# Kernel optimization log

Hardware: AMD Instinct MI355X
Metric: run time of the kernel (lower is better)

## Reference

```python
import jax, jax.numpy as jnp
import numpy as np
import math

L = 192
D = 128
H = 12
C = 24
EPS = 1e-5


def _layernorm(x, w, b):
    mu = jnp.mean(x, axis=-1, keepdims=True)
    var = jnp.var(x, axis=-1, keepdims=True)
    return (x - mu) * jax.lax.rsqrt(var + EPS) * w + b


def setup_inputs() -> dict:
    key = jax.random.key(0)
    ks = jax.random.split(key, 8)
    s = 0.02
    return {
        "z_": jax.random.normal(ks[0], (L, L, D), dtype=jnp.float32),
        "ln_w": jnp.ones((D,), jnp.float32),
        "ln_b": jnp.zeros((D,), jnp.float32),
        "Wq": jax.random.normal(ks[1], (D, H * C), jnp.float32) * s,
        "bq": jnp.zeros((H * C,), jnp.float32),
        "Wk": jax.random.normal(ks[2], (D, H * C), jnp.float32) * s,
        "bk": jnp.zeros((H * C,), jnp.float32),
        "Wv": jax.random.normal(ks[3], (D, H * C), jnp.float32) * s,
        "bv": jnp.zeros((H * C,), jnp.float32),
        "Wb": jax.random.normal(ks[4], (D, H), jnp.float32) * s,
        "bb": jnp.zeros((H,), jnp.float32),
        "Wg": jax.random.normal(ks[5], (D, H * C), jnp.float32) * s,
        "bg": jnp.zeros((H * C,), jnp.float32),
        "Wo": jax.random.normal(ks[6], (H * C, D), jnp.float32) * s,
        "bo": jnp.zeros((D,), jnp.float32),
    }


def reference(z_, ln_w, ln_b, Wq, bq, Wk, bk, Wv, bv, Wb, bb, Wg, bg, Wo, bo):
    sq_c = 1.0 / math.sqrt(C)
    z = _layernorm(z_, ln_w, ln_b)                     # [L, L, D]
    q = (z @ Wq + bq).reshape(L, L, H, C)
    k = (z @ Wk + bk).reshape(L, L, H, C)
    v = (z @ Wv + bv).reshape(L, L, H, C)
    bias = z @ Wb + bb                                 # [L, L, H]
    # att[b, l, kk, h] = sum_c q[b, l, h, c] * k[kk, b_==l? no: kk, b, h, c]
    att = jnp.einsum('blhc,kbhc->blkh', q, k) * sq_c
    # torch: b[None].permute(0,2,1,3) -> add bias[kk, l, h] broadcast over b
    att = att + jnp.transpose(bias, (1, 0, 2))[None, :, :, :]
    att = jax.nn.softmax(att, axis=2)
    o = jnp.einsum('blkh,klhc->blhc', att, v)          # [L, L, H, C]
    g = jax.nn.sigmoid((z @ Wg + bg).reshape(L, L, H, C))
    o = (g * o).reshape(L, L, H * C)
    return o @ Wo + bo
```

## Files before the change

### kernel.cpp

```cpp
#include <hip/hip_runtime.h>
#include <hip/hip_bf16.h>
#include <math.h>

typedef __hip_bfloat16 bf16;
typedef unsigned short u16;
typedef unsigned int u32;
typedef __attribute__((ext_vector_type(8))) short bf16x8;
typedef __attribute__((ext_vector_type(4))) float f32x4;

#define LL 36864

__device__ __forceinline__ float wave_sum(float v) {
#pragma unroll
  for (int m = 32; m; m >>= 1) v += __shfl_xor(v, m, 64);
  return v;
}

__device__ __forceinline__ float bf2f(u16 u) {
  union { float f; u32 u; } c; c.u = ((u32)u) << 16; return c.f;
}
__device__ __forceinline__ u16 f2bf(float f) {
  union { float f; u32 u; } c; c.f = f;
  u32 r = c.u + 0x7fffu + ((c.u >> 16) & 1u);
  return (u16)(r >> 16);
}

__global__ __launch_bounds__(256) void k_cvt(const float* __restrict__ Wq,
                                             const float* __restrict__ Wk,
                                             const float* __restrict__ Wv,
                                             const float* __restrict__ Wg,
                                             bf16* __restrict__ Wcat) {
  int u = blockIdx.x * 256 + threadIdx.x;
  if (u >= 18432) return;
  int jg = u >> 4, k0 = (u & 15) * 8;
  int sec = jg / 288, j = jg % 288;
  const float* W = sec == 0 ? Wq : sec == 1 ? Wk : sec == 2 ? Wv : Wg;
  u16 pk[8];
#pragma unroll
  for (int i = 0; i < 8; ++i) pk[i] = f2bf(W[(size_t)(k0 + i) * 288 + j]);
  *reinterpret_cast<uint4*>(&Wcat[(size_t)jg * 128 + k0]) = *reinterpret_cast<uint4*>(pk);
}

__global__ __launch_bounds__(256) void k_cvt2(const float* __restrict__ Wo,
                                              bf16* __restrict__ Wot) {
  int u = blockIdx.x * 256 + threadIdx.x;
  if (u >= 4608) return;
  int n = u / 36, k0 = (u % 36) * 8;
  u16 pk[8];
#pragma unroll
  for (int i = 0; i < 8; ++i) pk[i] = f2bf(Wo[(size_t)(k0 + i) * 128 + n]);
  *reinterpret_cast<uint4*>(&Wot[(size_t)n * 288 + k0]) = *reinterpret_cast<uint4*>(pk);
}

__global__ __launch_bounds__(256) void k_ln(const float* __restrict__ zin,
                                            const float* __restrict__ w_,
                                            const float* __restrict__ b_,
                                            bf16* __restrict__ zb) {
  int t = threadIdx.x;
  int wv = t >> 6, lane = t & 63;
  size_t m = (size_t)blockIdx.x * 4 + wv;
  const float2 v = *reinterpret_cast<const float2*>(&zin[m * 128 + lane * 2]);
  float s = wave_sum(v.x + v.y);
  float ss = wave_sum(v.x * v.x + v.y * v.y);
  float mean = s * (1.0f / 128.0f);
  float var = ss * (1.0f / 128.0f) - mean * mean;
  float rs = rsqrtf(var + 1e-5f);
  float o0 = (v.x - mean) * rs * w_[lane * 2] + b_[lane * 2];
  float o1 = (v.y - mean) * rs * w_[lane * 2 + 1] + b_[lane * 2 + 1];
  u32 pk = (u32)f2bf(o0) | ((u32)f2bf(o1) << 16);
  *reinterpret_cast<u32*>(&zb[m * 128 + lane * 2]) = pk;
}

__global__ __launch_bounds__(256) void k_bias(const bf16* __restrict__ zb,
                                              const float* __restrict__ Wb,
                                              const float* __restrict__ bbv,
                                              float* __restrict__ biasb) {
  int t = threadIdx.x;
  int w = t >> 6, lane = t & 63;
  int c15 = lane & 15, g = lane >> 4;
  int m0 = (blockIdx.x * 4 + w) * 16;
  f32x4 acc = (f32x4){0.f, 0.f, 0.f, 0.f};
#pragma unroll
  for (int kt = 0; kt < 4; ++kt) {
    bf16x8 a = *reinterpret_cast<const bf16x8*>(
        &zb[(size_t)(m0 + c15) * 128 + kt * 32 + g * 8]);
    u16 bp[8];
#pragma unroll
    for (int j = 0; j < 8; ++j)
      bp[j] = (c15 < 12) ? f2bf(Wb[(size_t)(kt * 32 + g * 8 + j) * 12 + c15]) : (u16)0;
    bf16x8 b = *reinterpret_cast<bf16x8*>(bp);
    acc = __builtin_amdgcn_mfma_f32_16x16x32_bf16(a, b, acc, 0, 0, 0);
  }
  if (c15 < 12) {
    int kk = m0 / 192, l0 = m0 % 192;
    int p = (kk & 15) * 12 + (kk >> 4);
    float bv = bbv[c15];
#pragma unroll
    for (int i = 0; i < 4; ++i) {
      int l = l0 + 4 * g + i;
      biasb[(size_t)c15 * LL + (size_t)l * 192 + p] = acc[i] + bv;
    }
  }
}

__global__ __launch_bounds__(256) void k_proj(const bf16* __restrict__ zb,
    const bf16* __restrict__ Wcat,
    const float* __restrict__ bq, const float* __restrict__ bk,
    const float* __restrict__ bv, const float* __restrict__ bg,
    bf16* __restrict__ q2, bf16* __restrict__ k2,
    bf16* __restrict__ vb, bf16* __restrict__ gbuf) {
  __shared__ __align__(16) u16 Sb[192 * 104];
  int t = threadIdx.x;
  int w = t >> 6, lane = t & 63;
  int c15 = lane & 15, g = lane >> 4;
  int wm = w & 1, wn = w >> 1;
  int bx = blockIdx.x, y = blockIdx.y;
  int sec = y / 3, h0 = (y % 3) * 4;
  int m0 = bx * 192;
  int jbase = y * 96;
  f32x4 acc[6][3];
#pragma unroll
  for (int mt = 0; mt < 6; ++mt)
#pragma unroll
    for (int nt = 0; nt < 3; ++nt) acc[mt][nt] = (f32x4){0.f, 0.f, 0.f, 0.f};
#pragma unroll
  for (int kt = 0; kt < 4; ++kt) {
    bf16x8 a[6], b[3];
#pragma unroll
    for (int mt = 0; mt < 6; ++mt)
      a[mt] = *reinterpret_cast<const bf16x8*>(
          &zb[(size_t)(m0 + wm * 96 + mt * 16 + c15) * 128 + kt * 32 + g * 8]);
#pragma unroll
    for (int nt = 0; nt < 3; ++nt)
      b[nt] = *reinterpret_cast<const bf16x8*>(
          &Wcat[(size_t)(jbase + wn * 48 + nt * 16 + c15) * 128 + kt * 32 + g * 8]);
#pragma unroll
    for (int mt = 0; mt < 6; ++mt)
#pragma unroll
      for (int nt = 0; nt < 3; ++nt)
        acc[mt][nt] = __builtin_amdgcn_mfma_f32_16x16x32_bf16(a[mt], b[nt], acc[mt][nt], 0, 0, 0);
  }
  const float* barr = sec == 0 ? bq : sec == 1 ? bk : sec == 2 ? bv : bg;
#pragma unroll
  for (int nt = 0; nt < 3; ++nt) {
    int col = wn * 48 + nt * 16 + c15;
    float bval = barr[(y % 3) * 96 + col];
#pragma unroll
    for (int mt = 0; mt < 6; ++mt) {
      int rbase = wm * 96 + mt * 16 + 4 * g;
#pragma unroll
      for (int i = 0; i < 4; ++i)
        Sb[(rbase + i) * 104 + col] = f2bf(acc[mt][nt][i] + bval);
    }
  }
  __syncthreads();
  if (sec == 0) {
    bf16* dst0 = q2 + ((size_t)bx * 12 + h0) * 4608;
    for (int u = t; u < 2304; u += 256) {
      int hl = u / 576, off = (u % 576) * 8;
      int ml = off / 24, c0 = off % 24;
      uint4 val = *reinterpret_cast<const uint4*>(&Sb[ml * 104 + hl * 24 + c0]);
      *reinterpret_cast<uint4*>(&dst0[(size_t)hl * 4608 + off]) = val;
    }
  } else if (sec == 3) {
    for (int u = t; u < 2304; u += 256) {
      int ml = u / 12, col = (u % 12) * 8;
      uint4 val = *reinterpret_cast<const uint4*>(&Sb[ml * 104 + col]);
      *reinterpret_cast<uint4*>(&gbuf[(size_t)(m0 + ml) * 288 + h0 * 24 + col]) = val;
    }
  } else {
    bf16* dst = (sec == 1) ? k2 : vb;
    for (int u = t; u < 2304; u += 256) {
      int hl = u / 576, off = (u % 576) * 8;
      int ml = off / 24, c0 = off % 24;
      uint4 val = *reinterpret_cast<const uint4*>(&Sb[ml * 104 + hl * 24 + c0]);
      *reinterpret_cast<uint4*>(
          &dst[(((size_t)ml * 12 + h0 + hl) * 192 + bx) * 24 + c0]) = val;
    }
  }
}

__global__ __launch_bounds__(256) void k_attpv(const bf16* __restrict__ q2,
    const bf16* __restrict__ k2, const float* __restrict__ biasb,
    const bf16* __restrict__ vbuf, const bf16* __restrict__ gbuf,
    bf16* __restrict__ Patt, const bf16* __restrict__ Ppv,
    bf16* __restrict__ ogb, int la0, int lp0, int NT, int NL) {
  __shared__ __align__(16) char ldsraw[25600];
  int t = threadIdx.x;
  int w = t >> 6, lane = t & 63;
  int c15 = lane & 15, g = lane >> 4;
  const float sq_c = 0.20412414523193154f;
  bool is_att = (la0 >= 0) && (lp0 < 0 || blockIdx.z == 0);
  if (is_att) {
    int x = blockIdx.x, h = blockIdx.y;
    if (x >= 48) return;
    int bq = x * 4 + w;
    int lbase = la0 + blockIdx.z * NT * 16;
    u16* Sb = reinterpret_cast<u16*>(ldsraw) + (size_t)w * 3200;
    const bf16* ks = &k2[((size_t)bq * 12 + h) * 4608];
    const float* bsrc = &biasb[(size_t)h * LL];
    for (int lt = 0; lt < NT; ++lt) {
      int l0 = lbase + lt * 16;
      const bf16* qs = &q2[(((size_t)bq * 12 + h) * 192 + l0) * 24];
      bf16x8 afr = {0, 0, 0, 0, 0, 0, 0, 0};
      if (g < 3) afr = *reinterpret_cast<const bf16x8*>(&qs[c15 * 24 + g * 8]);
      f32x4 acc[12];
#pragma unroll
      for (int ct = 0; ct < 12; ++ct) {
        bf16x8 bfr = {0, 0, 0, 0, 0, 0, 0, 0};
        if (g < 3) bfr = *reinterpret_cast<const bf16x8*>(&ks[(ct * 16 + c15) * 24 + g * 8]);
        acc[ct] = __builtin_amdgcn_mfma_f32_16x16x32_bf16(afr, bfr, (f32x4){0.f, 0.f, 0.f, 0.f}, 0, 0, 0);
      }
#pragma unroll
      for (int i = 0; i < 4; ++i) {
        const float* bT = &bsrc[(size_t)(l0 + 4 * g + i) * 192 + c15 * 12];
        float4 b0 = *reinterpret_cast<const float4*>(&bT[0]);
        float4 b1 = *reinterpret_cast<const float4*>(&bT[4]);
        float4 b2 = *reinterpret_cast<const float4*>(&bT[8]);
        float bb12[12] = {b0.x, b0.y, b0.z, b0.w, b1.x, b1.y, b1.z, b1.w,
                          b2.x, b2.y, b2.z, b2.w};
#pragma unroll
        for (int ct = 0; ct < 12; ++ct)
          acc[ct][i] = acc[ct][i] * sq_c + bb12[ct];
      }
      float inv[4];
#pragma unroll
      for (int i = 0; i < 4; ++i) {
        float mx = -1e30f;
#pragma unroll
        for (int ct = 0; ct < 12; ++ct) mx = fmaxf(mx, acc[ct][i]);
#pragma unroll
        for (int msk = 1; msk < 16; msk <<= 1) mx = fmaxf(mx, __shfl_xor(mx, msk, 64));
        float sm = 0.f;
#pragma unroll
        for (int ct = 0; ct < 12; ++ct) {
          float e = __expf(acc[ct][i] - mx);
          acc[ct][i] = e;
          sm += e;
        }
#pragma unroll
        for (int msk = 1; msk < 16; msk <<= 1) sm += __shfl_xor(sm, msk, 64);
        inv[i] = 1.0f / sm;
      }
#pragma unroll
      for (int i = 0; i < 4; ++i)
#pragma unroll
        for (int ct = 0; ct < 12; ++ct)
          Sb[(4 * g + i) * 200 + ct * 16 + c15] = f2bf(acc[ct][i] * inv[i]);
      int lrel = l0 - la0;
      for (int u = lane; u < 384; u += 64) {
        int lloc = u / 24, oct = u % 24;
        uint4 val = *reinterpret_cast<const uint4*>(&Sb[lloc * 200 + oct * 8]);
        *reinterpret_cast<uint4*>(
            &Patt[(((size_t)(lrel + lloc) * 12 + h) * 192 + bq) * 192 + oct * 8]) = val;
      }
    }
  } else {
    if (lp0 < 0) return;
    int x = blockIdx.x, h = blockIdx.y;
    if (x >= NL) return;
    u16* Vt = reinterpret_cast<u16*>(ldsraw);
    float* Ob = reinterpret_cast<float*>(ldsraw + 12800) + (size_t)w * 416;
    int l = lp0 + x;
    int lrel = x;
    const bf16* vs = &vbuf[((size_t)l * 12 + h) * 4608];
    for (int u = t; u < 576; u += 256) {
      int kk = u / 3, c0 = (u % 3) * 8;
      uint4 val = *reinterpret_cast<const uint4*>(&vs[kk * 24 + c0]);
      const u16* pv = reinterpret_cast<const u16*>(&val);
#pragma unroll
      for (int i = 0; i < 8; ++i) Vt[(c0 + i) * 200 + kk] = pv[i];
    }
    __syncthreads();
    bf16x8 bfr[6][2];
#pragma unroll
    for (int kt = 0; kt < 6; ++kt)
#pragma unroll
      for (int nt = 0; nt < 2; ++nt)
        bfr[kt][nt] = *reinterpret_cast<const bf16x8*>(
            &Vt[(nt * 16 + c15) * 200 + kt * 32 + g * 8]);
    const bf16* Ps = &Ppv[((size_t)lrel * 12 + h) * 36864];
#pragma unroll
    for (int mi = 0; mi < 3; ++mi) {
      int mt = w * 3 + mi;
      f32x4 acc0 = (f32x4){0.f, 0.f, 0.f, 0.f};
      f32x4 acc1 = (f32x4){0.f, 0.f, 0.f, 0.f};
#pragma unroll
      for (int kt = 0; kt < 6; ++kt) {
        bf16x8 a = *reinterpret_cast<const bf16x8*>(
            &Ps[(size_t)(mt * 16 + c15) * 192 + kt * 32 + g * 8]);
        acc0 = __builtin_amdgcn_mfma_f32_16x16x32_bf16(a, bfr[kt][0], acc0, 0, 0, 0);
        acc1 = __builtin_amdgcn_mfma_f32_16x16x32_bf16(a, bfr[kt][1], acc1, 0, 0, 0);
      }
#pragma unroll
      for (int i = 0; i < 4; ++i) {
        Ob[(4 * g + i) * 26 + c15] = acc0[i];
        if (c15 < 8) Ob[(4 * g + i) * 26 + 16 + c15] = acc1[i];
      }
      if (lane < 48) {
        int r = lane / 3, c0 = (lane % 3) * 8;
        int b = mt * 16 + r;
        size_t m = (size_t)b * 192 + l;
        uint4 gv4 = *reinterpret_cast<const uint4*>(&gbuf[m * 288 + h * 24 + c0]);
        const u16* gp = reinterpret_cast<const u16*>(&gv4);
        u16 opk[8];
#pragma unroll
        for (int i = 0; i < 8; ++i) {
          float av = Ob[r * 26 + c0 + i];
          float sg = 1.0f / (1.0f + __expf(-bf2f(gp[i])));
          opk[i] = f2bf(av * sg);
        }
        *reinterpret_cast<uint4*>(&ogb[m * 288 + h * 24 + c0]) = *reinterpret_cast<uint4*>(opk);
      }
    }
  }
}

__global__ __launch_bounds__(256) void k_out(const bf16* __restrict__ ogb,
                                             const bf16* __restrict__ Wot,
                                             const float* __restrict__ bo,
                                             float* __restrict__ out) {
  int t = threadIdx.x;
  int w = t >> 6, lane = t & 63;
  int c15 = lane & 15, g = lane >> 4;
  int m0 = blockIdx.x * 64;
  int mrow = m0 + w * 16 + c15;
  f32x4 acc[8];
#pragma unroll
  for (int nt = 0; nt < 8; ++nt) acc[nt] = (f32x4){0.f, 0.f, 0.f, 0.f};
#pragma unroll
  for (int kt = 0; kt < 9; ++kt) {
    bf16x8 a = *reinterpret_cast<const bf16x8*>(&ogb[(size_t)mrow * 288 + kt * 32 + g * 8]);
    bf16x8 b[8];
#pragma unroll
    for (int nt = 0; nt < 8; ++nt)
      b[nt] = *reinterpret_cast<const bf16x8*>(&Wot[(size_t)(nt * 16 + c15) * 288 + kt * 32 + g * 8]);
#pragma unroll
    for (int nt = 0; nt < 8; ++nt)
      acc[nt] = __builtin_amdgcn_mfma_f32_16x16x32_bf16(a, b[nt], acc[nt], 0, 0, 0);
  }
#pragma unroll
  for (int nt = 0; nt < 8; ++nt) {
    int n = nt * 16 + c15;
    float bval = bo[n];
#pragma unroll
    for (int i = 0; i < 4; ++i) {
      int m = m0 + w * 16 + 4 * g + i;
      out[(size_t)m * 128 + n] = acc[nt][i] + bval;
    }
  }
}

extern "C" void kernel_launch(void* const* d_in, const int* in_sizes, int n_in,
                              void* d_out, int out_size, void* d_ws, size_t ws_size,
                              hipStream_t stream) {
  const float* z_in = (const float*)d_in[0];
  const float* ln_w = (const float*)d_in[1];
  const float* ln_b = (const float*)d_in[2];
  const float* Wq   = (const float*)d_in[3];
  const float* bq   = (const float*)d_in[4];
  const float* Wk   = (const float*)d_in[5];
  const float* bk   = (const float*)d_in[6];
  const float* Wv   = (const float*)d_in[7];
  const float* bv   = (const float*)d_in[8];
  const float* Wb   = (const float*)d_in[9];
  const float* bb   = (const float*)d_in[10];
  const float* Wg   = (const float*)d_in[11];
  const float* bg   = (const float*)d_in[12];
  const float* Wo   = (const float*)d_in[13];
  const float* bo   = (const float*)d_in[14];
  float* out = (float*)d_out;

  char* ws = (char*)d_ws;

  if (ws_size >= 256573440ull) {
    bf16* q2    = (bf16*)(ws + 0);
    bf16* ogb   = (bf16*)(ws + 0);
    bf16* k2    = (bf16*)(ws + 21233664);
    bf16* vb    = (bf16*)(ws + 42467328);
    bf16* gbuf  = (bf16*)(ws + 63700992);
    float* biasb = (float*)(ws + 84934656);
    bf16* P     = (bf16*)(ws + 86704128);
    bf16* zb    = (bf16*)(ws + 86704128);
    bf16* Wcat  = (bf16*)(ws + 96141312);
    bf16* Wot   = (bf16*)(ws + 86704128);

    k_cvt<<<dim3(72), dim3(256), 0, stream>>>(Wq, Wk, Wv, Wg, Wcat);
    k_ln<<<dim3(9216), dim3(256), 0, stream>>>(z_in, ln_w, ln_b, zb);
    k_bias<<<dim3(576), dim3(256), 0, stream>>>(zb, Wb, bb, biasb);
    k_proj<<<dim3(192, 12), dim3(256), 0, stream>>>(zb, Wcat, bq, bk, bv, bg,
                                                    q2, k2, vb, gbuf);
    k_attpv<<<dim3(48, 12, 4), dim3(256), 0, stream>>>(
        q2, k2, biasb, vb, gbuf, P, P, ogb, 0, -1, 3, 192);
    k_attpv<<<dim3(192, 12, 1), dim3(256), 0, stream>>>(
        q2, k2, biasb, vb, gbuf, P, P, ogb, -1, 0, 12, 192);
    k_cvt2<<<dim3(18), dim3(256), 0, stream>>>(Wo, Wot);
    k_out<<<dim3(576), dim3(256), 0, stream>>>(ogb, Wot, bo, out);
    return;
  }

  bf16* q2    = (bf16*)(ws + 0);
  bf16* k2    = (bf16*)(ws + 21233664);
  bf16* vb    = (bf16*)(ws + 42467328);
  bf16* gbuf  = (bf16*)(ws + 63700992);
  bf16* ogb   = (bf16*)(ws + 84934656);
  bf16* zb    = (bf16*)(ws + 84934656);
  bf16* Wcat  = (bf16*)(ws + 94371840);
  float* biasb = (float*)(ws + 106168320);
  char* Pbase = ws + 107937792;
  bf16* Wot   = (bf16*)(ws + 107937792);

  k_cvt<<<dim3(72), dim3(256), 0, stream>>>(Wq, Wk, Wv, Wg, Wcat);
  k_ln<<<dim3(9216), dim3(256), 0, stream>>>(z_in, ln_w, ln_b, zb);
  k_bias<<<dim3(576), dim3(256), 0, stream>>>(zb, Wb, bb, biasb);
  k_proj<<<dim3(192, 12), dim3(256), 0, stream>>>(zb, Wcat, bq, bk, bv, bg,
                                                  q2, k2, vb, gbuf);
  const size_t PB = 107937792ull;
  int CL;
  if      (ws_size >= PB + 84934656ull)  CL = 48;
  else if (ws_size >= PB + 56623104ull)  CL = 32;
  else if (ws_size >= PB + 28311552ull)  CL = 16;
  else                                   CL = -16;
  if (CL > 0) {
    int nch = 192 / CL;
    size_t csz = (size_t)CL * 884736ull;
    bf16* P0 = (bf16*)Pbase;
    bf16* P1 = (bf16*)(Pbase + csz);
    int NT = CL / 16;
    for (int n = 0; n <= nch; ++n) {
      bf16* Pa = (n & 1) ? P1 : P0;
      bf16* Pp = ((n - 1) & 1) ? P1 : P0;
      int la = (n < nch) ? n * CL : -1;
      int lp = (n >= 1) ? (n - 1) * CL : -1;
      if (la >= 0 && lp >= 0)
        k_attpv<<<dim3(48 > CL ? 48 : CL, 12, 2), dim3(256), 0, stream>>>(
            q2, k2, biasb, vb, gbuf, Pa, Pp, ogb, la, lp, NT, CL);
      else if (la >= 0)
        k_attpv<<<dim3(48, 12, 1), dim3(256), 0, stream>>>(
            q2, k2, biasb, vb, gbuf, Pa, Pp, ogb, la, -1, NT, CL);
      else
        k_attpv<<<dim3(CL, 12, 1), dim3(256), 0, stream>>>(
            q2, k2, biasb, vb, gbuf, Pa, Pp, ogb, -1, lp, NT, CL);
    }
  } else {
    bf16* P0 = (bf16*)Pbase;
    for (int n = 0; n < 12; ++n) {
      k_attpv<<<dim3(48, 12, 1), dim3(256), 0, stream>>>(
          q2, k2, biasb, vb, gbuf, P0, P0, ogb, n * 16, -1, 1, 16);
      k_attpv<<<dim3(16, 12, 1), dim3(256), 0, stream>>>(
          q2, k2, biasb, vb, gbuf, P0, P0, ogb, -1, n * 16, 1, 16);
    }
  }
  k_cvt2<<<dim3(18), dim3(256), 0, stream>>>(Wo, Wot);
  k_out<<<dim3(576), dim3(256), 0, stream>>>(ogb, Wot, bo, out);
}
```

Baseline: 225.4 us.

## Pipeline attention and PV in three 64-row chunks with multi-slice launches

Removes the large-workspace path that computed the full attention matrix in one launch, then PV in a second. It is replaced by a chunked pipeline of 64-row chunks with two buffers. Attention for the next chunk runs in the same launch as PV for the previous chunk, with the split set by a new ZA parameter on the z dimension. The goal is to overlap the two phases, keep P traffic in a smaller working set, and cut the number of launches compared with the smaller-chunk paths. It needs a slightly different workspace threshold and adds fill and drain launches.

```diff
diff --git a/kernel.cpp b/kernel.cpp
--- a/kernel.cpp
+++ b/kernel.cpp
@@ -184,13 +184,13 @@
     const bf16* __restrict__ k2, const float* __restrict__ biasb,
     const bf16* __restrict__ vbuf, const bf16* __restrict__ gbuf,
     bf16* __restrict__ Patt, const bf16* __restrict__ Ppv,
-    bf16* __restrict__ ogb, int la0, int lp0, int NT, int NL) {
+    bf16* __restrict__ ogb, int la0, int lp0, int NT, int NL, int ZA) {
   __shared__ __align__(16) char ldsraw[25600];
   int t = threadIdx.x;
   int w = t >> 6, lane = t & 63;
   int c15 = lane & 15, g = lane >> 4;
   const float sq_c = 0.20412414523193154f;
-  bool is_att = (la0 >= 0) && (lp0 < 0 || blockIdx.z == 0);
+  bool is_att = ((int)blockIdx.z < ZA);
   if (is_att) {
     int x = blockIdx.x, h = blockIdx.y;
     if (x >= 48) return;
@@ -372,33 +372,6 @@
   float* out = (float*)d_out;
 
   char* ws = (char*)d_ws;
-
-  if (ws_size >= 256573440ull) {
-    bf16* q2    = (bf16*)(ws + 0);
-    bf16* ogb   = (bf16*)(ws + 0);
-    bf16* k2    = (bf16*)(ws + 21233664);
-    bf16* vb    = (bf16*)(ws + 42467328);
-    bf16* gbuf  = (bf16*)(ws + 63700992);
-    float* biasb = (float*)(ws + 84934656);
-    bf16* P     = (bf16*)(ws + 86704128);
-    bf16* zb    = (bf16*)(ws + 86704128);
-    bf16* Wcat  = (bf16*)(ws + 96141312);
-    bf16* Wot   = (bf16*)(ws + 86704128);
-
-    k_cvt<<<dim3(72), dim3(256), 0, stream>>>(Wq, Wk, Wv, Wg, Wcat);
-    k_ln<<<dim3(9216), dim3(256), 0, stream>>>(z_in, ln_w, ln_b, zb);
-    k_bias<<<dim3(576), dim3(256), 0, stream>>>(zb, Wb, bb, biasb);
-    k_proj<<<dim3(192, 12), dim3(256), 0, stream>>>(zb, Wcat, bq, bk, bv, bg,
-                                                    q2, k2, vb, gbuf);
-    k_attpv<<<dim3(48, 12, 4), dim3(256), 0, stream>>>(
-        q2, k2, biasb, vb, gbuf, P, P, ogb, 0, -1, 3, 192);
-    k_attpv<<<dim3(192, 12, 1), dim3(256), 0, stream>>>(
-        q2, k2, biasb, vb, gbuf, P, P, ogb, -1, 0, 12, 192);
-    k_cvt2<<<dim3(18), dim3(256), 0, stream>>>(Wo, Wot);
-    k_out<<<dim3(576), dim3(256), 0, stream>>>(ogb, Wot, bo, out);
-    return;
-  }
-
   bf16* q2    = (bf16*)(ws + 0);
   bf16* k2    = (bf16*)(ws + 21233664);
   bf16* vb    = (bf16*)(ws + 42467328);
@@ -409,46 +382,60 @@
   float* biasb = (float*)(ws + 106168320);
   char* Pbase = ws + 107937792;
   bf16* Wot   = (bf16*)(ws + 107937792);
+  const size_t PB = 107937792ull;
 
   k_cvt<<<dim3(72), dim3(256), 0, stream>>>(Wq, Wk, Wv, Wg, Wcat);
   k_ln<<<dim3(9216), dim3(256), 0, stream>>>(z_in, ln_w, ln_b, zb);
   k_bias<<<dim3(576), dim3(256), 0, stream>>>(zb, Wb, bb, biasb);
   k_proj<<<dim3(192, 12), dim3(256), 0, stream>>>(zb, Wcat, bq, bk, bv, bg,
                                                   q2, k2, vb, gbuf);
-  const size_t PB = 107937792ull;
-  int CL;
-  if      (ws_size >= PB + 84934656ull)  CL = 48;
-  else if (ws_size >= PB + 56623104ull)  CL = 32;
-  else if (ws_size >= PB + 28311552ull)  CL = 16;
-  else                                   CL = -16;
-  if (CL > 0) {
-    int nch = 192 / CL;
-    size_t csz = (size_t)CL * 884736ull;
+
+  if (ws_size >= PB + 113246208ull) {
     bf16* P0 = (bf16*)Pbase;
-    bf16* P1 = (bf16*)(Pbase + csz);
-    int NT = CL / 16;
-    for (int n = 0; n <= nch; ++n) {
-      bf16* Pa = (n & 1) ? P1 : P0;
-      bf16* Pp = ((n - 1) & 1) ? P1 : P0;
-      int la = (n < nch) ? n * CL : -1;
-      int lp = (n >= 1) ? (n - 1) * CL : -1;
-      if (la >= 0 && lp >= 0)
-        k_attpv<<<dim3(48 > CL ? 48 : CL, 12, 2), dim3(256), 0, stream>>>(
-            q2, k2, biasb, vb, gbuf, Pa, Pp, ogb, la, lp, NT, CL);
-      else if (la >= 0)
+    bf16* P1 = (bf16*)(Pbase + 56623104);
+    k_attpv<<<dim3(48, 12, 2), dim3(256), 0, stream>>>(
+        q2, k2, biasb, vb, gbuf, P0, P0, ogb, 0, -1, 2, 0, 2);
+    k_attpv<<<dim3(64, 12, 3), dim3(256), 0, stream>>>(
+        q2, k2, biasb, vb, gbuf, P1, P0, ogb, 64, 0, 2, 64, 2);
+    k_attpv<<<dim3(64, 12, 3), dim3(256), 0, stream>>>(
+        q2, k2, biasb, vb, gbuf, P0, P1, ogb, 128, 64, 2, 64, 2);
+    k_attpv<<<dim3(64, 12, 1), dim3(256), 0, stream>>>(
+        q2, k2, biasb, vb, gbuf, P0, P0, ogb, -1, 128, 0, 64, 0);
+  } else {
+    int CL;
+    if      (ws_size >= PB + 84934656ull)  CL = 48;
+    else if (ws_size >= PB + 56623104ull)  CL = 32;
+    else if (ws_size >= PB + 28311552ull)  CL = 16;
+    else                                   CL = -16;
+    if (CL > 0) {
+      int nch = 192 / CL;
+      size_t csz = (size_t)CL * 884736ull;
+      bf16* P0 = (bf16*)Pbase;
+      bf16* P1 = (bf16*)(Pbase + csz);
+      int NT = CL / 16;
+      for (int n = 0; n <= nch; ++n) {
+        bf16* Pa = (n & 1) ? P1 : P0;
+        bf16* Pp = ((n - 1) & 1) ? P1 : P0;
+        int la = (n < nch) ? n * CL : -1;
+        int lp = (n >= 1) ? (n - 1) * CL : -1;
+        if (la >= 0 && lp >= 0)
+          k_attpv<<<dim3(48 > CL ? 48 : CL, 12, 2), dim3(256), 0, stream>>>(
+              q2, k2, biasb, vb, gbuf, Pa, Pp, ogb, la, lp, NT, CL, 1);
+        else if (la >= 0)
+          k_attpv<<<dim3(48, 12, 1), dim3(256), 0, stream>>>(
+              q2, k2, biasb, vb, gbuf, Pa, Pp, ogb, la, -1, NT, CL, 1);
+        else
+          k_attpv<<<dim3(CL, 12, 1), dim3(256), 0, stream>>>(
+              q2, k2, biasb, vb, gbuf, Pa, Pp, ogb, -1, lp, NT, CL, 0);
+      }
+    } else {
+      bf16* P0 = (bf16*)Pbase;
+      for (int n = 0; n < 12; ++n) {
         k_attpv<<<dim3(48, 12, 1), dim3(256), 0, stream>>>(
-            q2, k2, biasb, vb, gbuf, Pa, Pp, ogb, la, -1, NT, CL);
-      else
-        k_attpv<<<dim3(CL, 12, 1), dim3(256), 0, stream>>>(
-            q2, k2, biasb, vb, gbuf, Pa, Pp, ogb, -1, lp, NT, CL);
-    }
-  } else {
-    bf16* P0 = (bf16*)Pbase;
-    for (int n = 0; n < 12; ++n) {
-      k_attpv<<<dim3(48, 12, 1), dim3(256), 0, stream>>>(
-          q2, k2, biasb, vb, gbuf, P0, P0, ogb, n * 16, -1, 1, 16);
-      k_attpv<<<dim3(16, 12, 1), dim3(256), 0, stream>>>(
-          q2, k2, biasb, vb, gbuf, P0, P0, ogb, -1, n * 16, 1, 16);
+            q2, k2, biasb, vb, gbuf, P0, P0, ogb, n * 16, -1, 1, 16, 1);
+        k_attpv<<<dim3(16, 12, 1), dim3(256), 0, stream>>>(
+            q2, k2, biasb, vb, gbuf, P0, P0, ogb, -1, n * 16, 1, 16, 0);
+      }
     }
   }
   k_cvt2<<<dim3(18), dim3(256), 0, stream>>>(Wo, Wot);
```

After: 239.5 us. 6.2% more time.
